# Performance work log

Hardware: AMD Instinct MI355X
Metric: run time of the kernel (lower is better)

Reference implementation:

```python
import jax, jax.numpy as jnp
import numpy as np

B, T, D, H = 2, 2048, 1024, 16
NEG = -65504.0


def setup_inputs() -> dict:
    key = jax.random.key(0)
    ks = jax.random.split(key, 12)
    std = float(np.sqrt(2.0 / (D + D)))  # xavier_normal for square weights
    inp = {
        'q': jax.random.normal(ks[0], (B, T, D), jnp.float32),
        'k': jax.random.normal(ks[1], (B, T, D), jnp.float32),
        'v': jax.random.normal(ks[2], (B, T, D), jnp.float32),
        'mask': jax.random.randint(ks[3], (B, T), 0, 2, jnp.int32),
        # weights stored as (in, out) so y = x @ W + b
        'Wq': jax.random.normal(ks[4], (D, D), jnp.float32) * std,
        'bq': jnp.zeros((D,), jnp.float32),
        'Wk': jax.random.normal(ks[5], (D, D), jnp.float32) * std,
        'bk': jnp.zeros((D,), jnp.float32),
        'Wv': jax.random.normal(ks[6], (D, D), jnp.float32) * std,
        'bv': jnp.zeros((D,), jnp.float32),
        'Wo': jax.random.normal(ks[7], (D, D), jnp.float32) * std,
        'bo': jnp.zeros((D,), jnp.float32),
    }
    return inp


def reference(q, k, v, mask, Wq, bq, Wk, bk, Wv, bv, Wo, bo):
    b, t, _ = q.shape
    dim_a = Wq.shape[1]
    dh = dim_a // H
    # projections, then split into heads: (b, t, H, dh)
    qh = (q @ Wq + bq).reshape(b, t, H, dh)
    kh = (k @ Wk + bk).reshape(b, t, H, dh)
    vh = (v @ Wv + bv).reshape(b, t, H, dh)
    # NOTE: module scales by 1/sqrt(dim_a) with the FULL dim_a, not per-head
    a = jnp.einsum('bthd,bshd->bhts', qh, kh) / jnp.sqrt(jnp.float32(dim_a))
    # 2D mask broadcasts over query positions: (b, 1, 1, t_keys)
    a = jnp.where(mask[:, None, None, :] == 0, NEG, a)
    a = jax.nn.softmax(a, axis=-1)  # dropout_prob=0 (eval mode)
    o = jnp.einsum('bhts,bshd->bthd', a, vh).reshape(b, t, dim_a)
    return o @ Wo + bo
```

## Files before the change

kernel.cpp:

```cpp
#include <hip/hip_runtime.h>
#include <hip/hip_bf16.h>
#include <math.h>

#define B_ 2
#define T_ 2048
#define D_ 1024
#define H_ 16
#define QSCALE (0.03125f * 1.44269504088896f)

typedef _Float16 f16;
using f16x4 = __attribute__((ext_vector_type(4))) _Float16;
using f16x8 = __attribute__((ext_vector_type(8))) _Float16;
using f32x4 = __attribute__((ext_vector_type(4))) float;

__device__ __forceinline__ void gl16(const void* g, void* l) {
  __builtin_amdgcn_global_load_lds(
      (__attribute__((address_space(1))) void*)g,
      (__attribute__((address_space(3))) void*)l, 16, 0, 0);
}

__device__ __forceinline__ unsigned lds_a32(const void* p) {
  return (unsigned)(size_t)(__attribute__((address_space(3))) const char*)p;
}

__global__ __launch_bounds__(256) void prep(
    const float* __restrict__ q, const float* __restrict__ k,
    const float* __restrict__ v, const int* __restrict__ mask,
    const float* __restrict__ Wq, const float* __restrict__ Wk,
    const float* __restrict__ Wv, const float* __restrict__ Wo,
    const float* __restrict__ bq, const float* __restrict__ bk,
    const float* __restrict__ bv, const float* __restrict__ bo,
    f16* __restrict__ xqkv, f16* __restrict__ Wt, float* __restrict__ bias,
    int* __restrict__ idx, int* __restrict__ inv, int* __restrict__ nk,
    f16* __restrict__ khc) {
  __shared__ float sh[64][65];
  const int bid = blockIdx.x;
  const int tid = threadIdx.x;

  if (bid < 6144) {
    const int z = bid / 2048;
    const float* src = (z == 0) ? q : (z == 1) ? k : v;
    const size_t i = ((size_t)(bid % 2048) * 256 + tid) * 8;
    float4 a = *(const float4*)(src + i);
    float4 b = *(const float4*)(src + i + 4);
    f16x8 o;
    o[0] = (f16)a.x; o[1] = (f16)a.y; o[2] = (f16)a.z; o[3] = (f16)a.w;
    o[4] = (f16)b.x; o[5] = (f16)b.y; o[6] = (f16)b.z; o[7] = (f16)b.w;
    *(f16x8*)(xqkv + (size_t)z * 4194304 + i) = o;
  } else if (bid < 7168) {
    const int id = bid - 6144;
    const int z = id >> 8;
    const int k0 = ((id >> 4) & 15) * 64, n0 = (id & 15) * 64;
    const float* W = (z == 0) ? Wq : (z == 1) ? Wk : (z == 2) ? Wv : Wo;
    const int r = tid >> 2, c0 = (tid & 3) * 16;
#pragma unroll
    for (int i = 0; i < 4; ++i)
      *(float4*)&sh[r][c0 + 4 * i] =
          *(const float4*)&W[(size_t)(k0 + r) * 1024 + n0 + c0 + 4 * i];
    __syncthreads();
    f16 tmp[16];
#pragma unroll
    for (int i = 0; i < 16; ++i) tmp[i] = (f16)sh[c0 + i][r];
    f16* dst = Wt + (size_t)z * 1048576 + (size_t)(n0 + r) * 1024 + k0 + c0;
    *(f16x8*)dst = *(f16x8*)&tmp[0];
    *(f16x8*)(dst + 8) = *(f16x8*)&tmp[8];
  } else if (bid < 7184) {
    const int i = (bid - 7168) * 256 + tid;
    const int z = i >> 10;
    const float* s = (z == 0) ? bq : (z == 1) ? bk : (z == 2) ? bv : bo;
    bias[i] = s[i & 1023];
  } else {
    const int b = bid - 7184;
    int* cnt = (int*)sh;
    int loc[8];
    int c = 0;
#pragma unroll
    for (int i = 0; i < 8; ++i) {
      loc[i] = mask[b * T_ + tid * 8 + i];
      c += loc[i];
    }
    cnt[tid] = c;
    __syncthreads();
    for (int off = 1; off < 256; off <<= 1) {
      int vsh = (tid >= off) ? cnt[tid - off] : 0;
      __syncthreads();
      cnt[tid] += vsh;
      __syncthreads();
    }
    int pos = cnt[tid] - c;
#pragma unroll
    for (int i = 0; i < 8; ++i) {
      const int t = tid * 8 + i;
      if (loc[i]) {
        idx[b * T_ + pos] = t;
        inv[b * T_ + t] = pos;
        ++pos;
      } else {
        inv[b * T_ + t] = -1;
      }
    }
    const int n = cnt[255];
    if (tid == 255) nk[b] = n;
    const int nkt = (n + 63) >> 6;
    const int npadrows = (nkt << 6) - n;
    uint4 z4 = {0u, 0u, 0u, 0u};
    f16* base = khc + ((size_t)b * T_ + n) * D_;
    for (int i = tid; i < npadrows * 128; i += 256)
      *(uint4*)(base + (size_t)i * 8) = z4;
  }
}

__global__ __launch_bounds__(256, 4) void gemm_r2(
    const f16* __restrict__ Xb, const f16* __restrict__ Wtb,
    const float* __restrict__ biasb, void* __restrict__ C0,
    void* __restrict__ C1, void* __restrict__ C2,
    const int* __restrict__ inv, float qscale) {
  __shared__ __align__(16) char lds[32768];
  const int z = blockIdx.z;
  const f16* X  = Xb  + (size_t)z * (4096 * 1024);
  const f16* Wt = Wtb + (size_t)z * (1024 * 1024);
  const float* bias = biasb + (size_t)z * 1024;
  f16* C = (f16*)((z == 0) ? C0 : (z == 1) ? C1 : C2);
  const float scl = (z == 0) ? qscale : 1.f;

  const int tid = threadIdx.x;
  const int wave = tid >> 6, lane = tid & 63;
  const int quad = lane >> 4, l16 = lane & 15;
  const int wm = wave & 1, wn = wave >> 1;
  const int m0 = blockIdx.y * 128, n0 = blockIdx.x * 128;

  const int r0 = tid >> 2;
  const int ssw = (tid & 3) ^ ((r0 >> 1) & 3);
  const f16* ap0 = X  + (size_t)(m0 + r0) * 1024 + ssw * 8;
  const f16* ap1 = ap0 + (size_t)64 * 1024;
  const f16* bp0 = Wt + (size_t)(n0 + r0) * 1024 + ssw * 8;
  const f16* bp1 = bp0 + (size_t)64 * 1024;
  char* al = lds + tid * 16;
  char* bl = lds + 8192 + tid * 16;

  const int sw16 = 16 * (quad ^ ((l16 >> 1) & 3));
  const unsigned a32 = lds_a32(lds + (64 * wm + l16) * 64 + sw16);
  const unsigned b32 = lds_a32(lds + 8192 + (64 * wn + l16) * 64 + sw16);

  f32x4 acc[4][4] = {};

#define R2_ISSUE(tt, sl) do {                                               \
    gl16(ap0 + (tt) * 32, al + (sl) * 16384);                               \
    gl16(ap1 + (tt) * 32, al + (sl) * 16384 + 4096);                        \
    gl16(bp0 + (tt) * 32, bl + (sl) * 16384);                               \
    gl16(bp1 + (tt) * 32, bl + (sl) * 16384 + 4096);                        \
    __builtin_amdgcn_sched_barrier(0);                                      \
  } while (0)

#define R2_WAIT(n) do {                                                     \
    asm volatile("s_waitcnt vmcnt(" #n ")");                                \
    __builtin_amdgcn_sched_barrier(0);                                      \
  } while (0)

#define R2_BAR() do {                                                       \
    __builtin_amdgcn_sched_barrier(0);                                      \
    asm volatile("s_barrier");                                              \
    __builtin_amdgcn_sched_barrier(0);                                      \
  } while (0)

#define R2_STR_(x) #x
#define R2_STR(x) R2_STR_(x)
#define DSR(dst, base, OFF)                                                 \
  asm volatile("ds_read_b128 %0, %1 offset:" R2_STR(OFF)                    \
               : "=v"(dst) : "v"(base))

#define R2_COMPUTE(sl) do {                                                 \
    R2_BAR();                                                               \
    const unsigned aa = a32 + (sl) * 16384;                                 \
    const unsigned bb = b32 + (sl) * 16384;                                 \
    f16x8 af[4], bf[4];                                                     \
    DSR(af[0], aa, 0);    DSR(af[1], aa, 1024);                             \
    DSR(bf[0], bb, 0);    DSR(bf[1], bb, 1024);                             \
    DSR(bf[2], bb, 2048); DSR(bf[3], bb, 3072);                             \
    DSR(af[2], aa, 2048); DSR(af[3], aa, 3072);                             \
    asm volatile("s_waitcnt lgkmcnt(2)");                                   \
    __builtin_amdgcn_sched_barrier(0);                                      \
    __builtin_amdgcn_s_setprio(1);                                          \
    _Pragma("unroll")                                                       \
    for (int mi = 0; mi < 2; ++mi)                                          \
      _Pragma("unroll")                                                     \
      for (int ni = 0; ni < 4; ++ni)                                        \
        acc[mi][ni] = __builtin_amdgcn_mfma_f32_16x16x32_f16(               \
            af[mi], bf[ni], acc[mi][ni], 0, 0, 0);                          \
    asm volatile("s_waitcnt lgkmcnt(0)");                                   \
    __builtin_amdgcn_sched_barrier(0);                                      \
    _Pragma("unroll")                                                       \
    for (int mi = 2; mi < 4; ++mi)                                          \
      _Pragma("unroll")                                                     \
      for (int ni = 0; ni < 4; ++ni)                                        \
        acc[mi][ni] = __builtin_amdgcn_mfma_f32_16x16x32_f16(               \
            af[mi], bf[ni], acc[mi][ni], 0, 0, 0);                          \
    __builtin_amdgcn_s_setprio(0);                                          \
    R2_BAR();                                                               \
  } while (0)

  R2_ISSUE(0, 0);
  for (int j = 0; j < 15; ++j) {
    R2_ISSUE(2 * j + 1, 1); R2_WAIT(4); R2_COMPUTE(0);
    R2_ISSUE(2 * j + 2, 0); R2_WAIT(4); R2_COMPUTE(1);
  }
  R2_ISSUE(31, 1); R2_WAIT(4); R2_COMPUTE(0);
  R2_WAIT(0); R2_COMPUTE(1);

#undef R2_ISSUE
#undef R2_WAIT
#undef R2_BAR
#undef DSR
#undef R2_STR
#undef R2_STR_
#undef R2_COMPUTE

  const int cm = m0 + 64 * wm + 4 * quad;
  const int cn = n0 + 64 * wn + l16;
  float bv[4];
#pragma unroll
  for (int ni = 0; ni < 4; ++ni) bv[ni] = bias[cn + 16 * ni];

  if (inv != nullptr && z == 1) {
    const int bb = m0 >> 11;
#pragma unroll
    for (int mi = 0; mi < 4; ++mi) {
#pragma unroll
      for (int r = 0; r < 4; ++r) {
        const int m = cm + 16 * mi + r;
        const int j = inv[m];
        if (j >= 0) {
          f16* row = C + ((size_t)(bb << 11) + j) * 1024;
#pragma unroll
          for (int ni = 0; ni < 4; ++ni)
            row[cn + 16 * ni] = (f16)(acc[mi][ni][r] + bv[ni]);
        }
      }
    }
  } else {
#pragma unroll
    for (int mi = 0; mi < 4; ++mi)
#pragma unroll
      for (int r = 0; r < 4; ++r) {
        f16* row = C + (size_t)(cm + 16 * mi + r) * 1024;
#pragma unroll
        for (int ni = 0; ni < 4; ++ni)
          row[cn + 16 * ni] = (f16)((acc[mi][ni][r] + bv[ni]) * scl);
      }
  }
}

template <int TM, typename OT>
__global__ __launch_bounds__(256) void gemm_bt(
    const f16* __restrict__ Xb, const f16* __restrict__ Wtb,
    const float* __restrict__ biasb, void* __restrict__ C0,
    void* __restrict__ C1, void* __restrict__ C2,
    const int* __restrict__ inv, int M, int N, int K, float qscale) {
  constexpr int FM = TM / 32;
  __shared__ __align__(16) f16 As[TM * 32];
  __shared__ __align__(16) f16 Bs[128 * 32];
  const int z = blockIdx.z;
  const f16* X  = Xb  + (size_t)z * M * K;
  const f16* Wt = Wtb + (size_t)z * N * K;
  const float* bias = biasb + (size_t)z * N;
  OT* C = (OT*)((z == 0) ? C0 : (z == 1) ? C1 : C2);
  const float scl = (z == 0) ? qscale : 1.f;

  const int tid = threadIdx.x;
  const int wave = tid >> 6, lane = tid & 63;
  const int quad = lane >> 4, l16 = lane & 15;
  const int wm = wave & 1, wn = wave >> 1;
  const int m0 = blockIdx.y * TM, n0 = blockIdx.x * 128;

  f32x4 acc[FM][4] = {};

  const f16* asrc = X  + (size_t)(m0 + (tid >> 2)) * K + (tid & 3) * 8;
  const f16* bsrc = Wt + (size_t)(n0 + (tid >> 2)) * K + (tid & 3) * 8;
  char* aldst = (char*)As + tid * 16;
  char* bldst = (char*)Bs + tid * 16;
  const size_t rstep = (size_t)64 * K;

  const int NK = K >> 5;
  for (int kt = 0; kt < NK; ++kt) {
    if (kt) __syncthreads();
    gl16(asrc, aldst);
    if constexpr (TM == 128) gl16(asrc + rstep, aldst + 4096);
    gl16(bsrc, bldst);
    gl16(bsrc + rstep, bldst + 4096);
    asrc += 32; bsrc += 32;
    __syncthreads();

    f16x8 af[FM], bf[4];
#pragma unroll
    for (int t = 0; t < FM; ++t)
      af[t] = *(const f16x8*)&As[((TM / 2) * wm + 16 * t + l16) * 32 + quad * 8];
#pragma unroll
    for (int t = 0; t < 4; ++t)
      bf[t] = *(const f16x8*)&Bs[(64 * wn + 16 * t + l16) * 32 + quad * 8];
#pragma unroll
    for (int i = 0; i < FM; ++i)
#pragma unroll
      for (int j = 0; j < 4; ++j)
        acc[i][j] = __builtin_amdgcn_mfma_f32_16x16x32_f16(af[i], bf[j], acc[i][j], 0, 0, 0);
  }

  const int cm = m0 + (TM / 2) * wm + 4 * quad;
  const int cn = n0 + 64 * wn + l16;
  float bv[4];
#pragma unroll
  for (int tn = 0; tn < 4; ++tn) bv[tn] = bias[cn + 16 * tn];

  if (inv != nullptr && z == 1) {
    const int bb = m0 >> 11;
#pragma unroll
    for (int tm = 0; tm < FM; ++tm) {
#pragma unroll
      for (int r = 0; r < 4; ++r) {
        const int m = cm + 16 * tm + r;
        const int j = inv[m];
        if (j >= 0) {
          OT* row = C + ((size_t)(bb << 11) + j) * N;
#pragma unroll
          for (int tn = 0; tn < 4; ++tn)
            row[cn + 16 * tn] = (OT)(acc[tm][tn][r] + bv[tn]);
        }
      }
    }
  } else {
#pragma unroll
    for (int tm = 0; tm < FM; ++tm)
#pragma unroll
      for (int r = 0; r < 4; ++r) {
        OT* row = C + (size_t)(cm + 16 * tm + r) * N;
#pragma unroll
        for (int tn = 0; tn < 4; ++tn)
          row[cn + 16 * tn] = (OT)((acc[tm][tn][r] + bv[tn]) * scl);
      }
  }
}

__global__ __launch_bounds__(256) void vtrans(
    const f16* __restrict__ vh, const int* __restrict__ idx,
    const int* __restrict__ nk, f16* __restrict__ vhT) {
  const int tt = blockIdx.x, bh = blockIdx.y;
  const int b = bh >> 4, h = bh & 15;
  const int n = nk[b];
  const int nkt = (n + 63) >> 6;
  if (tt >= nkt) return;
  __shared__ f16 t[64][72];
  const int tid = threadIdx.x;
  const int r = tid >> 2, cq = 16 * (tid & 3);

  const int j = tt * 64 + r;
  uint4 v0 = {0u, 0u, 0u, 0u}, v1 = {0u, 0u, 0u, 0u};
  if (j < n) {
    const int tsrc = idx[b * T_ + j];
    const uint4* src = (const uint4*)(vh + ((size_t)b * T_ + tsrc) * D_ + h * 64 + cq);
    v0 = src[0]; v1 = src[1];
  }
  *(uint4*)&t[r][cq]     = v0;
  *(uint4*)&t[r][cq + 8] = v1;
  __syncthreads();

  f16 tmp[16];
#pragma unroll
  for (int xx = 0; xx < 16; ++xx) {
    int x = (xx + r) & 15;
    tmp[x] = t[cq + x][r];
  }
  f16* dst = vhT + ((size_t)bh * 64 + r) * T_ + tt * 64 + cq;
  *(uint4*)&dst[0] = *(uint4*)&tmp[0];
  *(uint4*)&dst[8] = *(uint4*)&tmp[8];
}

__global__ __launch_bounds__(512) void attn_mfma(
    const f16* __restrict__ qh, const f16* __restrict__ khc,
    const f16* __restrict__ vhT, const int* __restrict__ nkd,
    f16* __restrict__ oat) {
  __shared__ f16 Ks[64][72];
  __shared__ f16 Vt[64][72];
  __shared__ f16 Ps[8][16][72];

  const int qt = blockIdx.x, bh = blockIdx.y;
  const int b = bh >> 4, h = bh & 15;
  const int tid = threadIdx.x;
  const int wave = tid >> 6, lane = tid & 63;
  const int quad = lane >> 4, l16 = lane & 15;
  const int sr = tid >> 3, sq = 8 * (tid & 7);

  const int n = nkd[b];
  const int nkt = (n + 63) >> 6;
  const int npad = (nkt << 6) - n;

  f16x8 qf[2];
  {
    const f16* qp = qh + ((size_t)(b * T_ + qt * 128 + wave * 16 + l16)) * D_ + h * 64 + quad * 8;
    qf[0] = *(const f16x8*)qp;
    qf[1] = *(const f16x8*)(qp + 32);
  }

  float lsum = 0.f;
  f32x4 o[4] = {};

  const f16* kbase = khc + (size_t)b * T_ * D_ + h * 64;
  const f16* vbase = vhT + ((size_t)bh * 64 + sr) * T_;

  uint4 kr, vr;
  auto load_kv = [&](int kt) {
    kr = *(const uint4*)(kbase + (size_t)(kt * 64 + sr) * D_ + sq);
    vr = *(const uint4*)(vbase + kt * 64 + sq);
  };
  if (nkt > 0) load_kv(0);

  for (int kt = 0; kt < nkt; ++kt) {
    *(uint4*)&Ks[sr][sq] = kr;
    *(uint4*)&Vt[sr][sq] = vr;
    __syncthreads();
    if (kt + 1 < nkt) load_kv(kt + 1);

#pragma unroll
    for (int tn = 0; tn < 4; ++tn) {
      f16x8 kf0 = *(const f16x8*)&Ks[16 * tn + l16][quad * 8];
      f16x8 kf1 = *(const f16x8*)&Ks[16 * tn + l16][32 + quad * 8];
      f32x4 s = {0.f, 0.f, 0.f, 0.f};
      s = __builtin_amdgcn_mfma_f32_16x16x32_f16(kf0, qf[0], s, 0, 0, 0);
      s = __builtin_amdgcn_mfma_f32_16x16x32_f16(kf1, qf[1], s, 0, 0, 0);
      float p0 = exp2f(s[0]), p1 = exp2f(s[1]);
      float p2 = exp2f(s[2]), p3 = exp2f(s[3]);
      lsum += (p0 + p1) + (p2 + p3);
      f16x4 pk;
      pk[0] = (f16)p0; pk[1] = (f16)p1; pk[2] = (f16)p2; pk[3] = (f16)p3;
      *(f16x4*)&Ps[wave][l16][16 * tn + 4 * quad] = pk;
    }

    f16x8 pf0 = *(const f16x8*)&Ps[wave][l16][quad * 8];
    f16x8 pf1 = *(const f16x8*)&Ps[wave][l16][32 + quad * 8];
#pragma unroll
    for (int t = 0; t < 4; ++t) {
      f16x8 vf0 = *(const f16x8*)&Vt[16 * t + l16][quad * 8];
      f16x8 vf1 = *(const f16x8*)&Vt[16 * t + l16][32 + quad * 8];
      o[t] = __builtin_amdgcn_mfma_f32_16x16x32_f16(pf0, vf0, o[t], 0, 0, 0);
      o[t] = __builtin_amdgcn_mfma_f32_16x16x32_f16(pf1, vf1, o[t], 0, 0, 0);
    }
    __syncthreads();
  }

  {
    float ls = lsum;
    ls += __shfl_xor(ls, 16);
    ls += __shfl_xor(ls, 32);
    ls -= (float)npad;
    const size_t orow = (size_t)(b * T_ + qt * 128 + wave * 16 + 4 * quad);
#pragma unroll
    for (int r = 0; r < 4; ++r) {
      const float iv = 1.f / __shfl(ls, 4 * quad + r);
#pragma unroll
      for (int t = 0; t < 4; ++t)
        oat[(orow + r) * D_ + h * 64 + 16 * t + l16] = (f16)(o[t][r] * iv);
    }
  }
}

extern "C" void kernel_launch(void* const* d_in, const int* in_sizes, int n_in,
                              void* d_out, int out_size, void* d_ws, size_t ws_size,
                              hipStream_t stream) {
  const float* q  = (const float*)d_in[0];
  const float* k  = (const float*)d_in[1];
  const float* v  = (const float*)d_in[2];
  const int* mask = (const int*)d_in[3];
  const float* Wq = (const float*)d_in[4];
  const float* bq = (const float*)d_in[5];
  const float* Wk = (const float*)d_in[6];
  const float* bk = (const float*)d_in[7];
  const float* Wv = (const float*)d_in[8];
  const float* bv = (const float*)d_in[9];
  const float* Wo = (const float*)d_in[10];
  const float* bo = (const float*)d_in[11];
  float* out = (float*)d_out;

  char* ws = (char*)d_ws;
  f16* xqkv  = (f16*)(ws);
  f16* Wt    = (f16*)(ws + 25165824);
  f16* qh    = (f16*)(ws + 33554432);
  f16* vh    = (f16*)(ws + 41943040);
  f16* khc   = (f16*)(ws + 50331648);
  float* bsw = (float*)(ws + 58720256);
  int* idx   = (int*)(ws + 58736640);
  int* inv   = (int*)(ws + 58753024);
  int* nk    = (int*)(ws + 58769408);
  f16* vhT   = (f16*)(ws);
  f16* oat   = (f16*)(ws + 8388608);

  const int M = B_ * T_;
  dim3 blk(256);

  prep<<<dim3(7186), blk, 0, stream>>>(q, k, v, mask, Wq, Wk, Wv, Wo,
                                       bq, bk, bv, bo, xqkv, Wt, bsw,
                                       idx, inv, nk, khc);

  gemm_r2<<<dim3(8, 32, 3), blk, 0, stream>>>(
      xqkv, Wt, bsw, qh, khc, vh, inv, QSCALE);

  vtrans<<<dim3(32, 32), blk, 0, stream>>>(vh, idx, nk, vhT);

  attn_mfma<<<dim3(16, 32), dim3(512), 0, stream>>>(qh, khc, vhT, nk, oat);

  gemm_bt<64, float><<<dim3(8, 64, 1), blk, 0, stream>>>(
      oat, Wt + 3145728, bsw + 3072, out, out, out, nullptr, M, D_, D_, 1.f);
}
```

Measured before the change: 223.6 us.

## Compact K/V input rows before projection and skip masked-out GEMM tiles

The mask scan moves into a tiny separate kernel that runs first. During fp16 conversion, the K and V inputs are scattered into compacted row order. The K/V projection GEMM then skips 128-row tiles beyond the valid key count and writes zeros into pad rows, and vtrans reads the compacted V directly without the idx gather. This cuts GEMM work for masked keys (about half the keys here, given the random mask) at the cost of an extra kernel launch and a serial dependency before prep1. It relies on masked keys contributing nothing; with the NEG fill that matches the reference unless every key in a batch is masked.

```diff
diff --git a/kernel.cpp b/kernel.cpp
--- a/kernel.cpp
+++ b/kernel.cpp
@@ -23,16 +23,44 @@
   return (unsigned)(size_t)(__attribute__((address_space(3))) const char*)p;
 }
 
-__global__ __launch_bounds__(256) void prep(
+__global__ __launch_bounds__(256) void prep0(
+    const int* __restrict__ mask, int* __restrict__ inv, int* __restrict__ nk) {
+  __shared__ int cnt[256];
+  const int b = blockIdx.x;
+  const int tid = threadIdx.x;
+  int loc[8];
+  int c = 0;
+#pragma unroll
+  for (int i = 0; i < 8; ++i) {
+    loc[i] = mask[b * T_ + tid * 8 + i];
+    c += loc[i];
+  }
+  cnt[tid] = c;
+  __syncthreads();
+  for (int off = 1; off < 256; off <<= 1) {
+    int vsh = (tid >= off) ? cnt[tid - off] : 0;
+    __syncthreads();
+    cnt[tid] += vsh;
+    __syncthreads();
+  }
+  int pos = cnt[tid] - c;
+#pragma unroll
+  for (int i = 0; i < 8; ++i) {
+    const int t = tid * 8 + i;
+    inv[b * T_ + t] = loc[i] ? pos : -1;
+    pos += loc[i];
+  }
+  if (tid == 255) nk[b] = cnt[255];
+}
+
+__global__ __launch_bounds__(256) void prep1(
     const float* __restrict__ q, const float* __restrict__ k,
-    const float* __restrict__ v, const int* __restrict__ mask,
+    const float* __restrict__ v, const int* __restrict__ inv,
     const float* __restrict__ Wq, const float* __restrict__ Wk,
     const float* __restrict__ Wv, const float* __restrict__ Wo,
     const float* __restrict__ bq, const float* __restrict__ bk,
     const float* __restrict__ bv, const float* __restrict__ bo,
-    f16* __restrict__ xqkv, f16* __restrict__ Wt, float* __restrict__ bias,
-    int* __restrict__ idx, int* __restrict__ inv, int* __restrict__ nk,
-    f16* __restrict__ khc) {
+    f16* __restrict__ xqkv, f16* __restrict__ Wt, float* __restrict__ bias) {
   __shared__ float sh[64][65];
   const int bid = blockIdx.x;
   const int tid = threadIdx.x;
@@ -42,11 +70,20 @@
     const float* src = (z == 0) ? q : (z == 1) ? k : v;
     const size_t i = ((size_t)(bid % 2048) * 256 + tid) * 8;
     float4 a = *(const float4*)(src + i);
-    float4 b = *(const float4*)(src + i + 4);
+    float4 b4 = *(const float4*)(src + i + 4);
     f16x8 o;
-    o[0] = (f16)a.x; o[1] = (f16)a.y; o[2] = (f16)a.z; o[3] = (f16)a.w;
-    o[4] = (f16)b.x; o[5] = (f16)b.y; o[6] = (f16)b.z; o[7] = (f16)b.w;
-    *(f16x8*)(xqkv + (size_t)z * 4194304 + i) = o;
+    o[0] = (f16)a.x;  o[1] = (f16)a.y;  o[2] = (f16)a.z;  o[3] = (f16)a.w;
+    o[4] = (f16)b4.x; o[5] = (f16)b4.y; o[6] = (f16)b4.z; o[7] = (f16)b4.w;
+    if (z == 0) {
+      *(f16x8*)(xqkv + i) = o;
+    } else {
+      const int tl = (int)(i >> 10);
+      const int bb = tl >> 11, t = tl & 2047;
+      const int j = inv[bb * T_ + t];
+      if (j >= 0)
+        *(f16x8*)(xqkv + (size_t)z * 4194304 +
+                  (((size_t)(bb * T_ + j)) << 10) + (i & 1023)) = o;
+    }
   } else if (bid < 7168) {
     const int id = bid - 6144;
     const int z = id >> 8;
@@ -64,49 +101,11 @@
     f16* dst = Wt + (size_t)z * 1048576 + (size_t)(n0 + r) * 1024 + k0 + c0;
     *(f16x8*)dst = *(f16x8*)&tmp[0];
     *(f16x8*)(dst + 8) = *(f16x8*)&tmp[8];
-  } else if (bid < 7184) {
+  } else {
     const int i = (bid - 7168) * 256 + tid;
     const int z = i >> 10;
     const float* s = (z == 0) ? bq : (z == 1) ? bk : (z == 2) ? bv : bo;
     bias[i] = s[i & 1023];
-  } else {
-    const int b = bid - 7184;
-    int* cnt = (int*)sh;
-    int loc[8];
-    int c = 0;
-#pragma unroll
-    for (int i = 0; i < 8; ++i) {
-      loc[i] = mask[b * T_ + tid * 8 + i];
-      c += loc[i];
-    }
-    cnt[tid] = c;
-    __syncthreads();
-    for (int off = 1; off < 256; off <<= 1) {
-      int vsh = (tid >= off) ? cnt[tid - off] : 0;
-      __syncthreads();
-      cnt[tid] += vsh;
-      __syncthreads();
-    }
-    int pos = cnt[tid] - c;
-#pragma unroll
-    for (int i = 0; i < 8; ++i) {
-      const int t = tid * 8 + i;
-      if (loc[i]) {
-        idx[b * T_ + pos] = t;
-        inv[b * T_ + t] = pos;
-        ++pos;
-      } else {
-        inv[b * T_ + t] = -1;
-      }
-    }
-    const int n = cnt[255];
-    if (tid == 255) nk[b] = n;
-    const int nkt = (n + 63) >> 6;
-    const int npadrows = (nkt << 6) - n;
-    uint4 z4 = {0u, 0u, 0u, 0u};
-    f16* base = khc + ((size_t)b * T_ + n) * D_;
-    for (int i = tid; i < npadrows * 128; i += 256)
-      *(uint4*)(base + (size_t)i * 8) = z4;
   }
 }
 
@@ -114,9 +113,17 @@
     const f16* __restrict__ Xb, const f16* __restrict__ Wtb,
     const float* __restrict__ biasb, void* __restrict__ C0,
     void* __restrict__ C1, void* __restrict__ C2,
-    const int* __restrict__ inv, float qscale) {
+    const int* __restrict__ nkd, float qscale) {
   __shared__ __align__(16) char lds[32768];
   const int z = blockIdx.z;
+  const int m0 = blockIdx.y * 128, n0 = blockIdx.x * 128;
+
+  if (z) {
+    const int nb = nkd[m0 >> 11];
+    const int lim = ((nb + 63) >> 6) << 6;
+    if ((m0 & 2047) >= lim) return;
+  }
+
   const f16* X  = Xb  + (size_t)z * (4096 * 1024);
   const f16* Wt = Wtb + (size_t)z * (1024 * 1024);
   const float* bias = biasb + (size_t)z * 1024;
@@ -127,7 +134,6 @@
   const int wave = tid >> 6, lane = tid & 63;
   const int quad = lane >> 4, l16 = lane & 15;
   const int wm = wave & 1, wn = wave >> 1;
-  const int m0 = blockIdx.y * 128, n0 = blockIdx.x * 128;
 
   const int r0 = tid >> 2;
   const int ssw = (tid & 3) ^ ((r0 >> 1) & 3);
@@ -221,31 +227,28 @@
 #pragma unroll
   for (int ni = 0; ni < 4; ++ni) bv[ni] = bias[cn + 16 * ni];
 
-  if (inv != nullptr && z == 1) {
-    const int bb = m0 >> 11;
-#pragma unroll
-    for (int mi = 0; mi < 4; ++mi) {
+  if (z == 0) {
+#pragma unroll
+    for (int mi = 0; mi < 4; ++mi)
+#pragma unroll
+      for (int r = 0; r < 4; ++r) {
+        f16* row = C + (size_t)(cm + 16 * mi + r) * 1024;
+#pragma unroll
+        for (int ni = 0; ni < 4; ++ni)
+          row[cn + 16 * ni] = (f16)((acc[mi][ni][r] + bv[ni]) * scl);
+      }
+  } else {
+    const int nb = nkd[m0 >> 11];
+#pragma unroll
+    for (int mi = 0; mi < 4; ++mi)
 #pragma unroll
       for (int r = 0; r < 4; ++r) {
         const int m = cm + 16 * mi + r;
-        const int j = inv[m];
-        if (j >= 0) {
-          f16* row = C + ((size_t)(bb << 11) + j) * 1024;
-#pragma unroll
-          for (int ni = 0; ni < 4; ++ni)
-            row[cn + 16 * ni] = (f16)(acc[mi][ni][r] + bv[ni]);
-        }
-      }
-    }
-  } else {
-#pragma unroll
-    for (int mi = 0; mi < 4; ++mi)
-#pragma unroll
-      for (int r = 0; r < 4; ++r) {
-        f16* row = C + (size_t)(cm + 16 * mi + r) * 1024;
+        const bool ok = (m & 2047) < nb;
+        f16* row = C + (size_t)m * 1024;
 #pragma unroll
         for (int ni = 0; ni < 4; ++ni)
-          row[cn + 16 * ni] = (f16)((acc[mi][ni][r] + bv[ni]) * scl);
+          row[cn + 16 * ni] = ok ? (f16)(acc[mi][ni][r] + bv[ni]) : (f16)0.f;
       }
   }
 }
@@ -254,17 +257,15 @@
 __global__ __launch_bounds__(256) void gemm_bt(
     const f16* __restrict__ Xb, const f16* __restrict__ Wtb,
     const float* __restrict__ biasb, void* __restrict__ C0,
-    void* __restrict__ C1, void* __restrict__ C2,
-    const int* __restrict__ inv, int M, int N, int K, float qscale) {
+    const int* __restrict__ unused, int M, int N, int K, float qscale) {
   constexpr int FM = TM / 32;
   __shared__ __align__(16) f16 As[TM * 32];
   __shared__ __align__(16) f16 Bs[128 * 32];
-  const int z = blockIdx.z;
-  const f16* X  = Xb  + (size_t)z * M * K;
-  const f16* Wt = Wtb + (size_t)z * N * K;
-  const float* bias = biasb + (size_t)z * N;
-  OT* C = (OT*)((z == 0) ? C0 : (z == 1) ? C1 : C2);
-  const float scl = (z == 0) ? qscale : 1.f;
+  const f16* X  = Xb;
+  const f16* Wt = Wtb;
+  const float* bias = biasb;
+  OT* C = (OT*)C0;
+  const float scl = qscale;
 
   const int tid = threadIdx.x;
   const int wave = tid >> 6, lane = tid & 63;
@@ -310,38 +311,20 @@
 #pragma unroll
   for (int tn = 0; tn < 4; ++tn) bv[tn] = bias[cn + 16 * tn];
 
-  if (inv != nullptr && z == 1) {
-    const int bb = m0 >> 11;
-#pragma unroll
-    for (int tm = 0; tm < FM; ++tm) {
-#pragma unroll
-      for (int r = 0; r < 4; ++r) {
-        const int m = cm + 16 * tm + r;
-        const int j = inv[m];
-        if (j >= 0) {
-          OT* row = C + ((size_t)(bb << 11) + j) * N;
-#pragma unroll
-          for (int tn = 0; tn < 4; ++tn)
-            row[cn + 16 * tn] = (OT)(acc[tm][tn][r] + bv[tn]);
-        }
-      }
+#pragma unroll
+  for (int tm = 0; tm < FM; ++tm)
+#pragma unroll
+    for (int r = 0; r < 4; ++r) {
+      OT* row = C + (size_t)(cm + 16 * tm + r) * N;
+#pragma unroll
+      for (int tn = 0; tn < 4; ++tn)
+        row[cn + 16 * tn] = (OT)((acc[tm][tn][r] + bv[tn]) * scl);
     }
-  } else {
-#pragma unroll
-    for (int tm = 0; tm < FM; ++tm)
-#pragma unroll
-      for (int r = 0; r < 4; ++r) {
-        OT* row = C + (size_t)(cm + 16 * tm + r) * N;
-#pragma unroll
-        for (int tn = 0; tn < 4; ++tn)
-          row[cn + 16 * tn] = (OT)((acc[tm][tn][r] + bv[tn]) * scl);
-      }
-  }
 }
 
 __global__ __launch_bounds__(256) void vtrans(
-    const f16* __restrict__ vh, const int* __restrict__ idx,
-    const int* __restrict__ nk, f16* __restrict__ vhT) {
+    const f16* __restrict__ vhc, const int* __restrict__ nk,
+    f16* __restrict__ vhT) {
   const int tt = blockIdx.x, bh = blockIdx.y;
   const int b = bh >> 4, h = bh & 15;
   const int n = nk[b];
@@ -354,8 +337,7 @@
   const int j = tt * 64 + r;
   uint4 v0 = {0u, 0u, 0u, 0u}, v1 = {0u, 0u, 0u, 0u};
   if (j < n) {
-    const int tsrc = idx[b * T_ + j];
-    const uint4* src = (const uint4*)(vh + ((size_t)b * T_ + tsrc) * D_ + h * 64 + cq);
+    const uint4* src = (const uint4*)(vhc + ((size_t)b * T_ + j) * D_ + h * 64 + cq);
     v0 = src[0]; v1 = src[1];
   }
   *(uint4*)&t[r][cq]     = v0;
@@ -482,29 +464,29 @@
   f16* xqkv  = (f16*)(ws);
   f16* Wt    = (f16*)(ws + 25165824);
   f16* qh    = (f16*)(ws + 33554432);
-  f16* vh    = (f16*)(ws + 41943040);
+  f16* vhc   = (f16*)(ws + 41943040);
   f16* khc   = (f16*)(ws + 50331648);
   float* bsw = (float*)(ws + 58720256);
-  int* idx   = (int*)(ws + 58736640);
-  int* inv   = (int*)(ws + 58753024);
-  int* nk    = (int*)(ws + 58769408);
+  int* inv   = (int*)(ws + 58736640);
+  int* nk    = (int*)(ws + 58753024);
   f16* vhT   = (f16*)(ws);
   f16* oat   = (f16*)(ws + 8388608);
 
   const int M = B_ * T_;
   dim3 blk(256);
 
-  prep<<<dim3(7186), blk, 0, stream>>>(q, k, v, mask, Wq, Wk, Wv, Wo,
-                                       bq, bk, bv, bo, xqkv, Wt, bsw,
-                                       idx, inv, nk, khc);
+  prep0<<<dim3(2), blk, 0, stream>>>(mask, inv, nk);
+
+  prep1<<<dim3(7184), blk, 0, stream>>>(q, k, v, inv, Wq, Wk, Wv, Wo,
+                                        bq, bk, bv, bo, xqkv, Wt, bsw);
 
   gemm_r2<<<dim3(8, 32, 3), blk, 0, stream>>>(
-      xqkv, Wt, bsw, qh, khc, vh, inv, QSCALE);
-
-  vtrans<<<dim3(32, 32), blk, 0, stream>>>(vh, idx, nk, vhT);
+      xqkv, Wt, bsw, qh, khc, vhc, nk, QSCALE);
+
+  vtrans<<<dim3(32, 32), blk, 0, stream>>>(vhc, nk, vhT);
 
   attn_mfma<<<dim3(16, 32), dim3(512), 0, stream>>>(qh, khc, vhT, nk, oat);
 
   gemm_bt<64, float><<<dim3(8, 64, 1), blk, 0, stream>>>(
-      oat, Wt + 3145728, bsw + 3072, out, out, out, nullptr, M, D_, D_, 1.f);
-}
+      oat, Wt + 3145728, bsw + 3072, out, nullptr, M, D_, D_, 1.f);
+}
```

New measurement: 224.0 us. No clear change (+0.2%).
